# Performance work log

Hardware: AMD Instinct MI355X
Metric: run time of the kernel (lower is better)

The kernel has to match this reference:

```python
import jax, jax.numpy as jnp
import numpy as np

N = 1_000_000
D_IN = 128
D_OUT = 128
SEGS = 8192


def setup_inputs() -> dict:
    key = jax.random.key(0)
    ks = jax.random.split(key, 8)
    x = jax.random.normal(ks[0], (N, D_IN), dtype=jnp.float32)
    index = jnp.sort(jax.random.randint(ks[1], (N,), 0, SEGS)).astype(jnp.int64)
    s = 0.02
    # gate_nn: Linear(D_IN, D_IN//2) -> ReLU -> Dropout(eval: id) -> Linear(D_IN//2, 1)
    W1 = jax.random.normal(ks[2], (D_IN, D_IN // 2), dtype=jnp.float32) * s
    b1 = jnp.zeros((D_IN // 2,), dtype=jnp.float32)
    W2 = jax.random.normal(ks[3], (D_IN // 2, 1), dtype=jnp.float32) * s
    b2 = jnp.zeros((1,), dtype=jnp.float32)
    # transform_nn: Linear(D_IN, D_OUT) -> ReLU -> Dropout(eval: id)
    Wt = jax.random.normal(ks[4], (D_IN, D_OUT), dtype=jnp.float32) * s
    bt = jnp.zeros((D_OUT,), dtype=jnp.float32)
    return {"x": x, "index": index, "W1": W1, "b1": b1, "W2": W2,
            "b2": b2, "Wt": Wt, "bt": bt, "dim_size": SEGS}


def reference(x, index, W1, b1, W2, b2, Wt, bt, dim_size):
    # Gate MLP -> per-node scalar score  [N]
    h = jax.nn.relu(x @ W1 + b1)
    gate = (h @ W2 + b2)[:, 0]
    # Segment softmax (PyG softmax: subtract segment max, exp, normalize)
    seg_max = jax.ops.segment_max(gate, index, num_segments=dim_size)
    e = jnp.exp(gate - seg_max[index])
    denom = jax.ops.segment_sum(e, index, num_segments=dim_size)
    alpha = e / (denom[index] + 1e-16)
    # Transform MLP then attention-weighted scatter sum  [dim_size, D_OUT]
    t = jax.nn.relu(x @ Wt + bt)
    out = jax.ops.segment_sum(alpha[:, None] * t, index, num_segments=dim_size)
    return out
```

## Files before the change

### kernel.cpp

```cpp
#include <hip/hip_runtime.h>
#include <hip/hip_bf16.h>
#include <math.h>

#define D   128
#define DH  64

typedef __attribute__((ext_vector_type(8))) __bf16 bf16x8;
typedef __attribute__((ext_vector_type(4))) float  f32x4;

union BF4 { __bf16 b[4]; ushort4 u; };

static __device__ __forceinline__ void bf16_split(float v, __bf16& hi, __bf16& lo) {
    hi = (__bf16)v;
    lo = (__bf16)(v - (float)hi);
}

__global__ void init_kernel(const float* __restrict__ Wt, const float* __restrict__ W1,
                            float* __restrict__ denom,
                            __bf16* __restrict__ WtT_hi, __bf16* __restrict__ WtT_lo,
                            __bf16* __restrict__ W1T_hi, __bf16* __restrict__ W1T_lo,
                            int nseg) {
    int i = blockIdx.x * 256 + threadIdx.x;
    if (i < nseg) denom[i] = 0.0f;
    if (i < D * D) {
        int j = i >> 7, k = i & (D - 1);
        __bf16 hi, lo; bf16_split(Wt[k * D + j], hi, lo);
        WtT_hi[j * D + k] = hi; WtT_lo[j * D + k] = lo;
    }
    if (i < DH * D) {
        int h = i >> 7, k = i & (D - 1);
        __bf16 hi, lo; bf16_split(W1[k * DH + h], hi, lo);
        W1T_hi[h * D + k] = hi; W1T_lo[h * D + k] = lo;
    }
}

static __device__ __forceinline__ void write_x_planes(
        const float4* xv, int tid, unsigned char* Ahi, unsigned char* Alo) {
    #pragma unroll
    for (int q = 0; q < 8; ++q) {
        int f = q * 256 + tid;
        int row = f >> 5, c4 = f & 31;
        BF4 h4, l4;
        bf16_split(xv[q].x, h4.b[0], l4.b[0]);
        bf16_split(xv[q].y, h4.b[1], l4.b[1]);
        bf16_split(xv[q].z, h4.b[2], l4.b[2]);
        bf16_split(xv[q].w, h4.b[3], l4.b[3]);
        int byte = (row * 256 + c4 * 8) ^ ((row & 7) << 4);
        *(ushort4*)(Ahi + byte) = h4.u;
        *(ushort4*)(Alo + byte) = l4.u;
    }
}

static __device__ __forceinline__ void load_x_chunk(
        const float4* __restrict__ xs, int chunk, int n_nodes, int tid, float4* xv) {
    #pragma unroll
    for (int q = 0; q < 8; ++q) {
        int f = q * 256 + tid;
        int node = chunk * 64 + (f >> 5);
        xv[q] = (node < n_nodes) ? xs[(size_t)chunk * 2048 + f]
                                 : make_float4(0.f, 0.f, 0.f, 0.f);
    }
}

__global__ __launch_bounds__(256, 2)
void fused_kernel(const float* __restrict__ x, const int* __restrict__ idx,
                  const __bf16* __restrict__ W1T_hi, const __bf16* __restrict__ W1T_lo,
                  const float* __restrict__ b1, const float* __restrict__ W2,
                  const float* __restrict__ b2,
                  const __bf16* __restrict__ WtT_hi, const __bf16* __restrict__ WtT_lo,
                  const float* __restrict__ bt,
                  float* __restrict__ denom, float* __restrict__ out,
                  int n_nodes, int nchunks) {
    __shared__ __align__(16) unsigned char Ahi[64 * 256], Alo[64 * 256];
    __shared__ float gpart[4][64];
    __shared__ float eld[64];
    __shared__ int   segs[2][64];
    int tid = threadIdx.x, lane = tid & 63, w = tid >> 6;
    int g = lane >> 4, l15 = lane & 15;

    bf16x8 B1h[4], B1l[4];
    {
        const __bf16* ph = W1T_hi + (size_t)(w * 16 + l15) * D;
        const __bf16* pl = W1T_lo + (size_t)(w * 16 + l15) * D;
        #pragma unroll
        for (int kk = 0; kk < 4; ++kk) {
            B1h[kk] = *(const bf16x8*)(ph + kk * 32 + g * 8);
            B1l[kk] = *(const bf16x8*)(pl + kk * 32 + g * 8);
        }
    }
    bf16x8 Bth[2][4], Btl[2][4];
    #pragma unroll
    for (int nt = 0; nt < 2; ++nt) {
        const __bf16* ph = WtT_hi + (size_t)((2 * w + nt) * 16 + l15) * D;
        const __bf16* pl = WtT_lo + (size_t)((2 * w + nt) * 16 + l15) * D;
        #pragma unroll
        for (int kk = 0; kk < 4; ++kk) {
            Bth[nt][kk] = *(const bf16x8*)(ph + kk * 32 + g * 8);
            Btl[nt][kk] = *(const bf16x8*)(pl + kk * 32 + g * 8);
        }
    }
    float b1v = b1[w * 16 + l15], w2v = W2[w * 16 + l15], b2v = b2[0];
    float btv[2] = { bt[(2 * w + 0) * 16 + l15], bt[(2 * w + 1) * 16 + l15] };
    const float4* xs = (const float4*)x;

    {
        int c0 = blockIdx.x;
        if (c0 < nchunks) {
            float4 xv[8];
            load_x_chunk(xs, c0, n_nodes, tid, xv);
            write_x_planes(xv, tid, Ahi, Alo);
            if (tid < 64) {
                int node = c0 * 64 + tid;
                segs[0][tid] = (node < n_nodes) ? idx[node] : 0;
            }
        }
    }

    int p = 0;
    for (int c = blockIdx.x; c < nchunks; c += gridDim.x, p ^= 1) {
        __syncthreads();
        int cn = c + gridDim.x;
        float4 xn[8]; int sgn = 0;
        if (cn < nchunks) {
            load_x_chunk(xs, cn, n_nodes, tid, xn);
            if (tid < 64) {
                int node = cn * 64 + tid;
                sgn = (node < n_nodes) ? idx[node] : 0;
            }
        }

        f32x4 gacc[4];
        #pragma unroll
        for (int rt = 0; rt < 4; ++rt) gacc[rt] = (f32x4){0.f, 0.f, 0.f, 0.f};
        #pragma unroll
        for (int kk = 0; kk < 4; ++kk) {
            #pragma unroll
            for (int rt = 0; rt < 4; ++rt) {
                int arow = rt * 16 + l15;
                int ab = (arow * 256 + kk * 64 + g * 16) ^ ((arow & 7) << 4);
                bf16x8 ah = *(const bf16x8*)(Ahi + ab);
                bf16x8 al = *(const bf16x8*)(Alo + ab);
                gacc[rt] = __builtin_amdgcn_mfma_f32_16x16x32_bf16(ah, B1h[kk], gacc[rt], 0, 0, 0);
                gacc[rt] = __builtin_amdgcn_mfma_f32_16x16x32_bf16(ah, B1l[kk], gacc[rt], 0, 0, 0);
                gacc[rt] = __builtin_amdgcn_mfma_f32_16x16x32_bf16(al, B1h[kk], gacc[rt], 0, 0, 0);
            }
        }
        #pragma unroll
        for (int rt = 0; rt < 4; ++rt) {
            #pragma unroll
            for (int r = 0; r < 4; ++r) {
                float pv = fmaxf(gacc[rt][r] + b1v, 0.f) * w2v;
                pv += __shfl_xor(pv, 1);
                pv += __shfl_xor(pv, 2);
                pv += __shfl_xor(pv, 4);
                pv += __shfl_xor(pv, 8);
                if (l15 == 0) gpart[w][rt * 16 + g * 4 + r] = pv;
            }
        }
        __syncthreads();

        f32x4 acc[4][2];
        #pragma unroll
        for (int rt = 0; rt < 4; ++rt)
            #pragma unroll
            for (int nt = 0; nt < 2; ++nt) acc[rt][nt] = (f32x4){0.f, 0.f, 0.f, 0.f};
        #pragma unroll
        for (int kk = 0; kk < 4; ++kk) {
            #pragma unroll
            for (int rt = 0; rt < 4; ++rt) {
                int arow = rt * 16 + l15;
                int ab = (arow * 256 + kk * 64 + g * 16) ^ ((arow & 7) << 4);
                bf16x8 ah = *(const bf16x8*)(Ahi + ab);
                bf16x8 al = *(const bf16x8*)(Alo + ab);
                #pragma unroll
                for (int nt = 0; nt < 2; ++nt) {
                    acc[rt][nt] = __builtin_amdgcn_mfma_f32_16x16x32_bf16(ah, Bth[nt][kk], acc[rt][nt], 0, 0, 0);
                    acc[rt][nt] = __builtin_amdgcn_mfma_f32_16x16x32_bf16(ah, Btl[nt][kk], acc[rt][nt], 0, 0, 0);
                    acc[rt][nt] = __builtin_amdgcn_mfma_f32_16x16x32_bf16(al, Bth[nt][kk], acc[rt][nt], 0, 0, 0);
                }
            }
        }

        if (tid < 64) {
            int node = c * 64 + tid;
            float gt = gpart[0][tid] + gpart[1][tid] + gpart[2][tid] + gpart[3][tid] + b2v;
            float e = (node < n_nodes) ? __expf(gt) : 0.f;
            eld[tid] = e;
            int ga = tid >> 4;
            int sa = segs[p][ga * 16], sb = segs[p][ga * 16 + 15];
            if (sa == sb) {
                float v = e;
                v += __shfl_xor(v, 1);
                v += __shfl_xor(v, 2);
                v += __shfl_xor(v, 4);
                v += __shfl_xor(v, 8);
                if ((tid & 15) == 0) atomicAdd(denom + sa, v);
            } else {
                atomicAdd(denom + segs[p][tid], e);
            }
        }
        __syncthreads();

        int s0 = segs[p][0], s63 = segs[p][63];
        if (s0 == s63) {
            float s[2] = {0.f, 0.f};
            #pragma unroll
            for (int rt = 0; rt < 4; ++rt)
                #pragma unroll
                for (int r = 0; r < 4; ++r) {
                    float a = eld[rt * 16 + g * 4 + r];
                    s[0] += a * fmaxf(acc[rt][0][r] + btv[0], 0.f);
                    s[1] += a * fmaxf(acc[rt][1][r] + btv[1], 0.f);
                }
            s[0] += __shfl_xor(s[0], 16); s[0] += __shfl_xor(s[0], 32);
            s[1] += __shfl_xor(s[1], 16); s[1] += __shfl_xor(s[1], 32);
            if (g == 0)      atomicAdd(&out[(size_t)s0 * D + (2 * w + 0) * 16 + l15], s[0]);
            else if (g == 1) atomicAdd(&out[(size_t)s0 * D + (2 * w + 1) * 16 + l15], s[1]);
        } else {
            #pragma unroll
            for (int rt = 0; rt < 4; ++rt) {
                int sa = segs[p][rt * 16], sb = segs[p][rt * 16 + 15];
                if (sa == sb) {
                    float s[2] = {0.f, 0.f};
                    #pragma unroll
                    for (int r = 0; r < 4; ++r) {
                        float a = eld[rt * 16 + g * 4 + r];
                        s[0] += a * fmaxf(acc[rt][0][r] + btv[0], 0.f);
                        s[1] += a * fmaxf(acc[rt][1][r] + btv[1], 0.f);
                    }
                    s[0] += __shfl_xor(s[0], 16); s[0] += __shfl_xor(s[0], 32);
                    s[1] += __shfl_xor(s[1], 16); s[1] += __shfl_xor(s[1], 32);
                    if (g == 0)      atomicAdd(&out[(size_t)sa * D + (2 * w + 0) * 16 + l15], s[0]);
                    else if (g == 1) atomicAdd(&out[(size_t)sa * D + (2 * w + 1) * 16 + l15], s[1]);
                } else {
                    #pragma unroll
                    for (int r = 0; r < 4; ++r) {
                        int row = rt * 16 + g * 4 + r;
                        int sg = segs[p][row];
                        float a = eld[row];
                        atomicAdd(&out[(size_t)sg * D + (2 * w + 0) * 16 + l15],
                                  a * fmaxf(acc[rt][0][r] + btv[0], 0.f));
                        atomicAdd(&out[(size_t)sg * D + (2 * w + 1) * 16 + l15],
                                  a * fmaxf(acc[rt][1][r] + btv[1], 0.f));
                    }
                }
            }
        }
        __syncthreads();

        if (cn < nchunks) {
            write_x_planes(xn, tid, Ahi, Alo);
            if (tid < 64) segs[p ^ 1][tid] = sgn;
        }
    }
}

__global__ void norm_kernel(float4* __restrict__ out4, const float* __restrict__ denom,
                            int n4) {
    int i = blockIdx.x * 256 + threadIdx.x;
    if (i >= n4) return;
    float rd = 1.0f / (denom[i >> 5] + 1e-16f);
    float4 v = out4[i];
    v.x *= rd; v.y *= rd; v.z *= rd; v.w *= rd;
    out4[i] = v;
}

extern "C" void kernel_launch(void* const* d_in, const int* in_sizes, int n_in,
                              void* d_out, int out_size, void* d_ws, size_t ws_size,
                              hipStream_t stream) {
    const float* x  = (const float*)d_in[0];
    const int* idx  = (const int*)d_in[1];
    const float* W1 = (const float*)d_in[2];
    const float* b1 = (const float*)d_in[3];
    const float* W2 = (const float*)d_in[4];
    const float* b2 = (const float*)d_in[5];
    const float* Wt = (const float*)d_in[6];
    const float* bt = (const float*)d_in[7];
    float* out = (float*)d_out;

    const int n_nodes = in_sizes[1];
    const int nseg = out_size / D;
    const int nchunks = (n_nodes + 63) / 64;

    char* base = (char*)d_ws;
    size_t off = 0;
    float* denom = (float*)(base + off);             off += (size_t)nseg * 4;
    off = (off + 511) & ~511ull;
    __bf16* WtT_hi = (__bf16*)(base + off);          off += (size_t)D * D * 2;
    __bf16* WtT_lo = (__bf16*)(base + off);          off += (size_t)D * D * 2;
    __bf16* W1T_hi = (__bf16*)(base + off);          off += (size_t)DH * D * 2;
    __bf16* W1T_lo = (__bf16*)(base + off);          off += (size_t)DH * D * 2;
    (void)ws_size;

    hipMemsetAsync(d_out, 0, (size_t)out_size * sizeof(float), stream);
    hipLaunchKernelGGL(init_kernel, dim3(64), dim3(256), 0, stream,
                       Wt, W1, denom, WtT_hi, WtT_lo, W1T_hi, W1T_lo, nseg);
    hipLaunchKernelGGL(fused_kernel, dim3(2048), dim3(256), 0, stream,
                       x, idx, W1T_hi, W1T_lo, b1, W2, b2,
                       WtT_hi, WtT_lo, bt, denom, out, n_nodes, nchunks);
    int n4 = out_size / 4;
    hipLaunchKernelGGL(norm_kernel, dim3((n4 + 255) / 256), dim3(256), 0, stream,
                       (float4*)d_out, denom, n4);
}
```

Before: 885.4 us.

## Fuse gate and transform MFMA loops, drop W1 low plane, replace LDS exchange with shuffles

The gate and transform matmuls now run in one K loop, so each A fragment is read from LDS once instead of twice. The W1 bf16 low-plane correction term is removed, which cuts gate MFMAs from three to two per tile at some cost in gate precision. The per-node exp value is shared with wave shuffles instead of an LDS array, which removes two __syncthreads, and the launch bounds are raised to three blocks per CU. The fused loop keeps more accumulators and weight fragments live at once, so register pressure may cause spills under the tighter occupancy target.

```diff
diff --git a/kernel.cpp b/kernel.cpp
--- a/kernel.cpp
+++ b/kernel.cpp
@@ -18,7 +18,7 @@
 __global__ void init_kernel(const float* __restrict__ Wt, const float* __restrict__ W1,
                             float* __restrict__ denom,
                             __bf16* __restrict__ WtT_hi, __bf16* __restrict__ WtT_lo,
-                            __bf16* __restrict__ W1T_hi, __bf16* __restrict__ W1T_lo,
+                            __bf16* __restrict__ W1T_hi,
                             int nseg) {
     int i = blockIdx.x * 256 + threadIdx.x;
     if (i < nseg) denom[i] = 0.0f;
@@ -29,8 +29,7 @@
     }
     if (i < DH * D) {
         int h = i >> 7, k = i & (D - 1);
-        __bf16 hi, lo; bf16_split(W1[k * DH + h], hi, lo);
-        W1T_hi[h * D + k] = hi; W1T_lo[h * D + k] = lo;
+        W1T_hi[h * D + k] = (__bf16)W1[k * DH + h];
     }
 }
 
@@ -62,9 +61,9 @@
     }
 }
 
-__global__ __launch_bounds__(256, 2)
+__global__ __launch_bounds__(256, 3)
 void fused_kernel(const float* __restrict__ x, const int* __restrict__ idx,
-                  const __bf16* __restrict__ W1T_hi, const __bf16* __restrict__ W1T_lo,
+                  const __bf16* __restrict__ W1T_hi,
                   const float* __restrict__ b1, const float* __restrict__ W2,
                   const float* __restrict__ b2,
                   const __bf16* __restrict__ WtT_hi, const __bf16* __restrict__ WtT_lo,
@@ -73,20 +72,16 @@
                   int n_nodes, int nchunks) {
     __shared__ __align__(16) unsigned char Ahi[64 * 256], Alo[64 * 256];
     __shared__ float gpart[4][64];
-    __shared__ float eld[64];
     __shared__ int   segs[2][64];
     int tid = threadIdx.x, lane = tid & 63, w = tid >> 6;
     int g = lane >> 4, l15 = lane & 15;
 
-    bf16x8 B1h[4], B1l[4];
+    bf16x8 B1h[4];
     {
         const __bf16* ph = W1T_hi + (size_t)(w * 16 + l15) * D;
-        const __bf16* pl = W1T_lo + (size_t)(w * 16 + l15) * D;
-        #pragma unroll
-        for (int kk = 0; kk < 4; ++kk) {
+        #pragma unroll
+        for (int kk = 0; kk < 4; ++kk)
             B1h[kk] = *(const bf16x8*)(ph + kk * 32 + g * 8);
-            B1l[kk] = *(const bf16x8*)(pl + kk * 32 + g * 8);
-        }
     }
     bf16x8 Bth[2][4], Btl[2][4];
     #pragma unroll
@@ -130,8 +125,13 @@
         }
 
         f32x4 gacc[4];
-        #pragma unroll
-        for (int rt = 0; rt < 4; ++rt) gacc[rt] = (f32x4){0.f, 0.f, 0.f, 0.f};
+        f32x4 acc[4][2];
+        #pragma unroll
+        for (int rt = 0; rt < 4; ++rt) {
+            gacc[rt] = (f32x4){0.f, 0.f, 0.f, 0.f};
+            #pragma unroll
+            for (int nt = 0; nt < 2; ++nt) acc[rt][nt] = (f32x4){0.f, 0.f, 0.f, 0.f};
+        }
         #pragma unroll
         for (int kk = 0; kk < 4; ++kk) {
             #pragma unroll
@@ -141,10 +141,16 @@
                 bf16x8 ah = *(const bf16x8*)(Ahi + ab);
                 bf16x8 al = *(const bf16x8*)(Alo + ab);
                 gacc[rt] = __builtin_amdgcn_mfma_f32_16x16x32_bf16(ah, B1h[kk], gacc[rt], 0, 0, 0);
-                gacc[rt] = __builtin_amdgcn_mfma_f32_16x16x32_bf16(ah, B1l[kk], gacc[rt], 0, 0, 0);
                 gacc[rt] = __builtin_amdgcn_mfma_f32_16x16x32_bf16(al, B1h[kk], gacc[rt], 0, 0, 0);
-            }
-        }
+                #pragma unroll
+                for (int nt = 0; nt < 2; ++nt) {
+                    acc[rt][nt] = __builtin_amdgcn_mfma_f32_16x16x32_bf16(ah, Bth[nt][kk], acc[rt][nt], 0, 0, 0);
+                    acc[rt][nt] = __builtin_amdgcn_mfma_f32_16x16x32_bf16(ah, Btl[nt][kk], acc[rt][nt], 0, 0, 0);
+                    acc[rt][nt] = __builtin_amdgcn_mfma_f32_16x16x32_bf16(al, Bth[nt][kk], acc[rt][nt], 0, 0, 0);
+                }
+            }
+        }
+
         #pragma unroll
         for (int rt = 0; rt < 4; ++rt) {
             #pragma unroll
@@ -159,34 +165,12 @@
         }
         __syncthreads();
 
-        f32x4 acc[4][2];
-        #pragma unroll
-        for (int rt = 0; rt < 4; ++rt)
-            #pragma unroll
-            for (int nt = 0; nt < 2; ++nt) acc[rt][nt] = (f32x4){0.f, 0.f, 0.f, 0.f};
-        #pragma unroll
-        for (int kk = 0; kk < 4; ++kk) {
-            #pragma unroll
-            for (int rt = 0; rt < 4; ++rt) {
-                int arow = rt * 16 + l15;
-                int ab = (arow * 256 + kk * 64 + g * 16) ^ ((arow & 7) << 4);
-                bf16x8 ah = *(const bf16x8*)(Ahi + ab);
-                bf16x8 al = *(const bf16x8*)(Alo + ab);
-                #pragma unroll
-                for (int nt = 0; nt < 2; ++nt) {
-                    acc[rt][nt] = __builtin_amdgcn_mfma_f32_16x16x32_bf16(ah, Bth[nt][kk], acc[rt][nt], 0, 0, 0);
-                    acc[rt][nt] = __builtin_amdgcn_mfma_f32_16x16x32_bf16(ah, Btl[nt][kk], acc[rt][nt], 0, 0, 0);
-                    acc[rt][nt] = __builtin_amdgcn_mfma_f32_16x16x32_bf16(al, Bth[nt][kk], acc[rt][nt], 0, 0, 0);
-                }
-            }
-        }
-
-        if (tid < 64) {
-            int node = c * 64 + tid;
-            float gt = gpart[0][tid] + gpart[1][tid] + gpart[2][tid] + gpart[3][tid] + b2v;
-            float e = (node < n_nodes) ? __expf(gt) : 0.f;
-            eld[tid] = e;
-            int ga = tid >> 4;
+        float gt = gpart[0][lane] + gpart[1][lane] + gpart[2][lane] + gpart[3][lane] + b2v;
+        int node0 = c * 64 + lane;
+        float e = (node0 < n_nodes) ? __expf(gt) : 0.f;
+
+        if (w == 0) {
+            int ga = lane >> 4;
             int sa = segs[p][ga * 16], sb = segs[p][ga * 16 + 15];
             if (sa == sb) {
                 float v = e;
@@ -194,12 +178,11 @@
                 v += __shfl_xor(v, 2);
                 v += __shfl_xor(v, 4);
                 v += __shfl_xor(v, 8);
-                if ((tid & 15) == 0) atomicAdd(denom + sa, v);
+                if ((lane & 15) == 0) atomicAdd(denom + sa, v);
             } else {
-                atomicAdd(denom + segs[p][tid], e);
-            }
-        }
-        __syncthreads();
+                atomicAdd(denom + segs[p][lane], e);
+            }
+        }
 
         int s0 = segs[p][0], s63 = segs[p][63];
         if (s0 == s63) {
@@ -208,7 +191,7 @@
             for (int rt = 0; rt < 4; ++rt)
                 #pragma unroll
                 for (int r = 0; r < 4; ++r) {
-                    float a = eld[rt * 16 + g * 4 + r];
+                    float a = __shfl(e, rt * 16 + g * 4 + r);
                     s[0] += a * fmaxf(acc[rt][0][r] + btv[0], 0.f);
                     s[1] += a * fmaxf(acc[rt][1][r] + btv[1], 0.f);
                 }
@@ -224,7 +207,7 @@
                     float s[2] = {0.f, 0.f};
                     #pragma unroll
                     for (int r = 0; r < 4; ++r) {
-                        float a = eld[rt * 16 + g * 4 + r];
+                        float a = __shfl(e, rt * 16 + g * 4 + r);
                         s[0] += a * fmaxf(acc[rt][0][r] + btv[0], 0.f);
                         s[1] += a * fmaxf(acc[rt][1][r] + btv[1], 0.f);
                     }
@@ -237,7 +220,7 @@
                     for (int r = 0; r < 4; ++r) {
                         int row = rt * 16 + g * 4 + r;
                         int sg = segs[p][row];
-                        float a = eld[row];
+                        float a = __shfl(e, row);
                         atomicAdd(&out[(size_t)sg * D + (2 * w + 0) * 16 + l15],
                                   a * fmaxf(acc[rt][0][r] + btv[0], 0.f));
                         atomicAdd(&out[(size_t)sg * D + (2 * w + 1) * 16 + l15],
@@ -246,7 +229,6 @@
                 }
             }
         }
-        __syncthreads();
 
         if (cn < nchunks) {
             write_x_planes(xn, tid, Ahi, Alo);
@@ -289,14 +271,13 @@
     __bf16* WtT_hi = (__bf16*)(base + off);          off += (size_t)D * D * 2;
     __bf16* WtT_lo = (__bf16*)(base + off);          off += (size_t)D * D * 2;
     __bf16* W1T_hi = (__bf16*)(base + off);          off += (size_t)DH * D * 2;
-    __bf16* W1T_lo = (__bf16*)(base + off);          off += (size_t)DH * D * 2;
     (void)ws_size;
 
     hipMemsetAsync(d_out, 0, (size_t)out_size * sizeof(float), stream);
     hipLaunchKernelGGL(init_kernel, dim3(64), dim3(256), 0, stream,
-                       Wt, W1, denom, WtT_hi, WtT_lo, W1T_hi, W1T_lo, nseg);
+                       Wt, W1, denom, WtT_hi, WtT_lo, W1T_hi, nseg);
     hipLaunchKernelGGL(fused_kernel, dim3(2048), dim3(256), 0, stream,
-                       x, idx, W1T_hi, W1T_lo, b1, W2, b2,
+                       x, idx, W1T_hi, b1, W2, b2,
                        WtT_hi, WtT_lo, bt, denom, out, n_nodes, nchunks);
     int n4 = out_size / 4;
     hipLaunchKernelGGL(norm_kernel, dim3((n4 + 255) / 256), dim3(256), 0, stream,
```

Result: slower. 1.239 ms (+39.9%).
